# Performance work log

Measured on AMD Instinct MI355X. Metric: run time of the kernel, lower is better.

## Reference

```python
import jax, jax.numpy as jnp
import numpy as np

N = 50000
NEG_SLOPE = 0.2


def add_self_loops(edge_index, n):
    loops = jnp.arange(n, dtype=edge_index.dtype)
    return jnp.concatenate([edge_index, jnp.stack([loops, loops])], axis=1)


def gat_layer(x, edge_index, W, a_src, a_dst, b, heads, ch):
    # x: [N, F_in], W: [F_in, heads*ch], a_src/a_dst: [heads, ch], b: [heads*ch]
    n = x.shape[0]
    src, dst = edge_index[0], edge_index[1]
    h = (x @ W).reshape(n, heads, ch)                      # [N, H, C]
    alpha_src = jnp.sum(h * a_src, axis=-1)                # [N, H]
    alpha_dst = jnp.sum(h * a_dst, axis=-1)                # [N, H]
    e = jax.nn.leaky_relu(alpha_src[src] + alpha_dst[dst], NEG_SLOPE)  # [E, H]
    # segment softmax over incoming edges of each destination node
    m = jax.ops.segment_max(e, dst, num_segments=n)        # [N, H]
    ex = jnp.exp(e - m[dst])                               # [E, H]
    denom = jax.ops.segment_sum(ex, dst, num_segments=n)   # [N, H]
    alpha = ex / (denom[dst] + 1e-16)                      # [E, H]
    msg = h[src] * alpha[:, :, None]                       # [E, H, C]
    out = jax.ops.segment_sum(msg, dst, num_segments=n)    # [N, H, C]
    return out.reshape(n, heads * ch) + b


def setup_inputs() -> dict:
    key = jax.random.key(0)
    ks = jax.random.split(key, 12)
    input_dim, hidden_dim, output_dim, heads = 128, 32, 64, 4
    E = 1600000
    x = jax.random.normal(ks[0], (N, input_dim), dtype=jnp.float32)
    edge_index = jax.random.randint(ks[1], (2, E), 0, N, dtype=jnp.int64)
    s1 = 1.0 / np.sqrt(input_dim)
    s2 = 1.0 / np.sqrt(hidden_dim * heads)
    W1 = jax.random.uniform(ks[2], (input_dim, heads * hidden_dim), jnp.float32, -s1, s1)
    a_src1 = jax.random.uniform(ks[3], (heads, hidden_dim), jnp.float32, -s1, s1)
    a_dst1 = jax.random.uniform(ks[4], (heads, hidden_dim), jnp.float32, -s1, s1)
    b1 = jnp.zeros((heads * hidden_dim,), jnp.float32)
    W2 = jax.random.uniform(ks[5], (heads * hidden_dim, output_dim), jnp.float32, -s2, s2)
    a_src2 = jax.random.uniform(ks[6], (1, output_dim), jnp.float32, -s2, s2)
    a_dst2 = jax.random.uniform(ks[7], (1, output_dim), jnp.float32, -s2, s2)
    b2 = jnp.zeros((output_dim,), jnp.float32)
    return {"x": x, "edge_index": edge_index,
            "W1": W1, "a_src1": a_src1, "a_dst1": a_dst1, "b1": b1,
            "W2": W2, "a_src2": a_src2, "a_dst2": a_dst2, "b2": b2}


def reference(x, edge_index, W1, a_src1, a_dst1, b1, W2, a_src2, a_dst2, b2):
    n = x.shape[0]
    ei = add_self_loops(edge_index, n)
    h = gat_layer(x, ei, W1, a_src1, a_dst1, b1, heads=4, ch=32)
    h = jax.nn.relu(h)
    out = gat_layer(h, ei, W2, a_src2, a_dst2, b2, heads=1, ch=64)
    return out
```

## Files before the change

kernel.cpp:

```cpp
#include <hip/hip_runtime.h>
#include <hip/hip_bf16.h>
#include <hip/hip_fp16.h>


#define LRELU_SLOPE 0.2f
#define NBMAX 200
#define NBLK  512
#define BCAP  16384
#define CAPIMG 16384

typedef _Float16 f16x8 __attribute__((ext_vector_type(8)));
typedef float f32x4 __attribute__((ext_vector_type(4)));


__global__ __launch_bounds__(256) void hist_kernel(const int* __restrict__ ei_dst,
                                                   int* __restrict__ hist, int E, int chunk) {
    __shared__ int h[NBMAX];
    int t = threadIdx.x;
    for (int i = t; i < NBMAX; i += 256) h[i] = 0;
    __syncthreads();
    int begin = blockIdx.x * chunk;
    int endE = min(E, begin + chunk);
    for (int e = begin + t; e < endE; e += 256) atomicAdd(&h[ei_dst[e] >> 8], 1);
    __syncthreads();
    for (int i = t; i < NBMAX; i += 256) hist[i * NBLK + blockIdx.x] = h[i];
}

__global__ __launch_bounds__(512) void bucket_scan_kernel(int* __restrict__ hist,
                                                          int* __restrict__ gfill) {
    __shared__ int buf[2][NBLK];
    int b = blockIdx.x, t = threadIdx.x;
    buf[0][t] = hist[b * NBLK + t];
    __syncthreads();
    int pi = 0;
#pragma unroll
    for (int off = 1; off < NBLK; off <<= 1) {
        int v = buf[pi][t];
        if (t >= off) v += buf[pi][t - off];
        buf[pi ^ 1][t] = v;
        __syncthreads();
        pi ^= 1;
    }
    hist[b * NBLK + t] = (t == 0) ? 0 : buf[pi][t - 1];
    if (t == 0) gfill[b] = buf[pi][NBLK - 1];
}

__global__ __launch_bounds__(256) void scatter2_kernel(const int* __restrict__ ei_src,
                                                       const int* __restrict__ ei_dst,
                                                       const int* __restrict__ hist,
                                                       unsigned int* __restrict__ records,
                                                       int E, int chunk) {
    __shared__ int base[NBMAX];
    __shared__ int lcnt[NBMAX];
    int t = threadIdx.x;
    for (int i = t; i < NBMAX; i += 256) {
        base[i] = hist[i * NBLK + blockIdx.x];
        lcnt[i] = 0;
    }
    __syncthreads();
    int begin = blockIdx.x * chunk;
    int endE = min(E, begin + chunk);
    for (int e = begin + t; e < endE; e += 256) {
        int s = ei_src[e], d = ei_dst[e];
        int bkt = d >> 8;
        unsigned int rec = (unsigned int)d | ((unsigned int)s << 16);
        int r = atomicAdd(&lcnt[bkt], 1);
        records[(size_t)bkt * BCAP + base[bkt] + r] = rec;
    }
}

__global__ __launch_bounds__(256) void scan_blocksums_kernel(const int* __restrict__ gfill,
                                                             int* __restrict__ bsums,
                                                             int* __restrict__ row_ptr,
                                                             int nblocks, int n, int total) {
    __shared__ int buf[2][256];
    int t = threadIdx.x;
    int v0 = 0;
    if (t < nblocks) v0 = gfill[t] + min(256, n - (t << 8));
    buf[0][t] = v0;
    __syncthreads();
    int pi = 0;
#pragma unroll
    for (int off = 1; off < 256; off <<= 1) {
        int v = buf[pi][t];
        if (t >= off) v += buf[pi][t - off];
        buf[pi ^ 1][t] = v;
        __syncthreads();
        pi ^= 1;
    }
    if (t < nblocks) bsums[t] = (t == 0) ? 0 : buf[pi][t - 1];
    if (t == 0) row_ptr[n] = total;
}

__global__ __launch_bounds__(256) void csr_build_kernel(const unsigned int* __restrict__ records,
                                                        const int* __restrict__ gfill,
                                                        const int* __restrict__ bsums,
                                                        int* __restrict__ row_ptr,
                                                        unsigned short* __restrict__ col,
                                                        int N) {
    __shared__ int cnt[256];
    __shared__ int buf[2][256];
    __shared__ unsigned short img[CAPIMG];
    __shared__ int lfill[256];
    int t = threadIdx.x, b = blockIdx.x;
    int gi = (b << 8) + t;
    bool valid = gi < N;
    cnt[t] = valid ? 1 : 0;
    __syncthreads();
    int c = gfill[b];
    const unsigned int* r = records + (size_t)b * BCAP;
    for (int i = t; i < c; i += 256) atomicAdd(&cnt[r[i] & 255], 1);
    __syncthreads();
    int d = cnt[t];
    buf[0][t] = d;
    __syncthreads();
    int pi = 0;
#pragma unroll
    for (int off = 1; off < 256; off <<= 1) {
        int v = buf[pi][t];
        if (t >= off) v += buf[pi][t - off];
        buf[pi ^ 1][t] = v;
        __syncthreads();
        pi ^= 1;
    }
    int rbase = bsums[b];
    int nvalid = min(256, N - (b << 8));
    int size = c + max(nvalid, 0);
    bool lds = (size <= CAPIMG);
    if (valid) {
        int local = buf[pi][t] - d;
        row_ptr[gi] = rbase + local;
        lfill[t] = local + 1;
        if (lds) img[local] = (unsigned short)gi;
        else col[rbase + local] = (unsigned short)gi;
    }
    __syncthreads();
    for (int i = t; i < c; i += 256) {
        unsigned int rec = r[i];
        int d8 = rec & 255;
        unsigned short s = (unsigned short)(rec >> 16);
        int p = atomicAdd(&lfill[d8], 1);
        if (lds) img[p] = s;
        else col[rbase + p] = s;
    }
    __syncthreads();
    if (lds) {
        for (int i = t; i < size; i += 256) col[rbase + i] = img[i];
    }
}


__global__ __launch_bounds__(256) void gemm1_mfma_kernel(const float* __restrict__ X,
                                                         const float* __restrict__ W,
                                                         __half* __restrict__ outh,
                                                         const float* __restrict__ a_src,
                                                         const float* __restrict__ a_dst,
                                                         float* __restrict__ as_out,
                                                         float* __restrict__ ad_out, int nrows) {
    constexpr int KP = 136;
    __shared__ _Float16 wlds[128 * KP];
    int t = threadIdx.x;
    int wv = t >> 6, lane = t & 63;
    int quad = lane >> 4, m16 = lane & 15;
    for (int i = t; i < 4096; i += 256) {
        int k = i >> 5;
        int n0 = (i & 31) << 2;
        float4 v = *(const float4*)(W + k * 128 + n0);
        wlds[(n0 + 0) * KP + k] = (_Float16)v.x;
        wlds[(n0 + 1) * KP + k] = (_Float16)v.y;
        wlds[(n0 + 2) * KP + k] = (_Float16)v.z;
        wlds[(n0 + 3) * KP + k] = (_Float16)v.w;
    }
    __syncthreads();

    int row = blockIdx.x * 64 + wv * 16 + m16;
    int rowC = min(row, nrows - 1);
    const float* xp = X + (size_t)rowC * 128;

    f32x4 acc[8];
#pragma unroll
    for (int nt = 0; nt < 8; ++nt) acc[nt] = (f32x4)0.f;

    for (int kt = 0; kt < 128; kt += 32) {
        float4 v0 = *(const float4*)(xp + kt + quad * 8);
        float4 v1 = *(const float4*)(xp + kt + quad * 8 + 4);
        f16x8 af;
        af[0] = (_Float16)v0.x; af[1] = (_Float16)v0.y;
        af[2] = (_Float16)v0.z; af[3] = (_Float16)v0.w;
        af[4] = (_Float16)v1.x; af[5] = (_Float16)v1.y;
        af[6] = (_Float16)v1.z; af[7] = (_Float16)v1.w;
#pragma unroll
        for (int nt = 0; nt < 8; ++nt) {
            f16x8 bf = *(const f16x8*)(&wlds[(nt * 16 + m16) * KP + kt + quad * 8]);
            acc[nt] = __builtin_amdgcn_mfma_f32_16x16x32_f16(af, bf, acc[nt], 0, 0, 0);
        }
    }

    float aS[8], aD[8];
#pragma unroll
    for (int nt = 0; nt < 8; ++nt) {
        aS[nt] = a_src[nt * 16 + m16];
        aD[nt] = a_dst[nt * 16 + m16];
    }
    int rowBaseW = blockIdx.x * 64 + wv * 16;
#pragma unroll
    for (int r = 0; r < 4; ++r) {
        int orow = rowBaseW + quad * 4 + r;
        bool ov = orow < nrows;
        if (ov) {
#pragma unroll
            for (int nt = 0; nt < 8; ++nt)
                outh[(size_t)orow * 128 + nt * 16 + m16] = __float2half(acc[nt][r]);
        }
#pragma unroll
        for (int h = 0; h < 4; ++h) {
            float ss = acc[2 * h][r] * aS[2 * h] + acc[2 * h + 1][r] * aS[2 * h + 1];
            float dd = acc[2 * h][r] * aD[2 * h] + acc[2 * h + 1][r] * aD[2 * h + 1];
#pragma unroll
            for (int o = 1; o < 16; o <<= 1) {
                ss += __shfl_xor(ss, o, 64);
                dd += __shfl_xor(dd, o, 64);
            }
            if (ov && m16 == h) {
                as_out[orow * 4 + h] = ss;
                ad_out[orow * 4 + h] = dd;
            }
        }
    }
}


__global__ __launch_bounds__(256) void gemm2_mfma_kernel(const __half* __restrict__ Xh,
                                                         const float* __restrict__ W,
                                                         __half* __restrict__ outh,
                                                         const float* __restrict__ a_src,
                                                         const float* __restrict__ a_dst,
                                                         float* __restrict__ as_out,
                                                         float* __restrict__ ad_out, int nrows) {
    constexpr int KP = 136;
    __shared__ _Float16 wlds[64 * KP];
    int t = threadIdx.x;
    int wv = t >> 6, lane = t & 63;
    int quad = lane >> 4, m16 = lane & 15;
    for (int i = t; i < 2048; i += 256) {
        int k = i >> 4;
        int n0 = (i & 15) << 2;
        float4 v = *(const float4*)(W + k * 64 + n0);
        wlds[(n0 + 0) * KP + k] = (_Float16)v.x;
        wlds[(n0 + 1) * KP + k] = (_Float16)v.y;
        wlds[(n0 + 2) * KP + k] = (_Float16)v.z;
        wlds[(n0 + 3) * KP + k] = (_Float16)v.w;
    }
    __syncthreads();

    int row = blockIdx.x * 64 + wv * 16 + m16;
    int rowC = min(row, nrows - 1);
    const _Float16* xp = (const _Float16*)Xh + (size_t)rowC * 128;

    f32x4 acc[4];
#pragma unroll
    for (int nt = 0; nt < 4; ++nt) acc[nt] = (f32x4)0.f;

    for (int kt = 0; kt < 128; kt += 32) {
        f16x8 af = *(const f16x8*)(xp + kt + quad * 8);
#pragma unroll
        for (int nt = 0; nt < 4; ++nt) {
            f16x8 bf = *(const f16x8*)(&wlds[(nt * 16 + m16) * KP + kt + quad * 8]);
            acc[nt] = __builtin_amdgcn_mfma_f32_16x16x32_f16(af, bf, acc[nt], 0, 0, 0);
        }
    }

    float aS[4], aD[4];
#pragma unroll
    for (int nt = 0; nt < 4; ++nt) {
        aS[nt] = a_src[nt * 16 + m16];
        aD[nt] = a_dst[nt * 16 + m16];
    }
    int rowBaseW = blockIdx.x * 64 + wv * 16;
#pragma unroll
    for (int r = 0; r < 4; ++r) {
        int orow = rowBaseW + quad * 4 + r;
        bool ov = orow < nrows;
        if (ov) {
#pragma unroll
            for (int nt = 0; nt < 4; ++nt)
                outh[(size_t)orow * 64 + nt * 16 + m16] = __float2half(acc[nt][r]);
        }
        float ss = 0.f, dd = 0.f;
#pragma unroll
        for (int nt = 0; nt < 4; ++nt) {
            ss = fmaf(acc[nt][r], aS[nt], ss);
            dd = fmaf(acc[nt][r], aD[nt], dd);
        }
#pragma unroll
        for (int o = 1; o < 16; o <<= 1) {
            ss += __shfl_xor(ss, o, 64);
            dd += __shfl_xor(dd, o, 64);
        }
        if (ov && m16 == 0) {
            as_out[orow] = ss;
            ad_out[orow] = dd;
        }
    }
}


__global__ __launch_bounds__(256) void agg1_kernel(const __half* __restrict__ h1h,
                                                   const float* __restrict__ asrc,
                                                   const float* __restrict__ adst,
                                                   const int* __restrict__ row_ptr,
                                                   const unsigned short* __restrict__ col,
                                                   const float* __restrict__ b1,
                                                   __half* __restrict__ out, int n) {
    int wave = threadIdx.x >> 6;
    int lane = threadIdx.x & 63;
    int node = blockIdx.x * 4 + wave;
    if (node >= n) return;
    int g = lane >> 4;
    int c16 = lane & 15;
    int headA = c16 >> 2;
    int hp1 = lane & 3;
    int j16 = lane >> 2;
    float ad1 = adst[node * 4 + hp1];
    int start = row_ptr[node], end = row_ptr[node + 1];
    float acc[8];
#pragma unroll
    for (int k = 0; k < 8; ++k) acc[k] = 0.f;
    float s = 0.f;
    const _Float16* hp = (const _Float16*)h1h;
    for (int base = start; base < end; base += 64) {
        int idx = base + lane;
        int cnt = min(64, end - base);
        int myS = (idx < end) ? (int)col[idx] : 0;
        float pr[4];
#pragma unroll
        for (int e = 0; e < 4; ++e) {
            int j = e * 16 + j16;
            int srcj = __shfl(myS, j, 64);
            float ev = asrc[srcj * 4 + hp1] + ad1;
            ev = (ev > 0.f) ? ev : LRELU_SLOPE * ev;
            pr[e] = (j < cnt) ? __expf(ev) : 0.f;
        }
#pragma unroll
        for (int e = 0; e < 4; ++e) {
            int ebase = e << 4;
            if (ebase < cnt) {
                float pre = pr[e];
                int lim = min(ebase + 16, cnt);
                for (int j0 = ebase; j0 < lim; j0 += 4) {
                    int edge = j0 + g;
                    unsigned src = (unsigned)__shfl(myS, edge, 64);
                    float p = __shfl(pre, ((edge & 15) << 2) + headA, 64);
                    f16x8 hv = *(const f16x8*)(hp + ((size_t)src << 7) + (c16 << 3));
#pragma unroll
                    for (int k = 0; k < 8; ++k) acc[k] = fmaf(p, (float)hv[k], acc[k]);
                    s += p;
                }
            }
        }
    }
    s += __shfl_xor(s, 16, 64);
    s += __shfl_xor(s, 32, 64);
#pragma unroll
    for (int k = 0; k < 8; ++k) {
        acc[k] += __shfl_xor(acc[k], 16, 64);
        acc[k] += __shfl_xor(acc[k], 32, 64);
    }
    if (g == 0) {
        float inv = 1.f / (s + 1e-16f);
        float4 bb0 = ((const float4*)b1)[c16 * 2];
        float4 bb1 = ((const float4*)b1)[c16 * 2 + 1];
        f16x8 o;
        o[0] = (_Float16)fmaxf(acc[0] * inv + bb0.x, 0.f);
        o[1] = (_Float16)fmaxf(acc[1] * inv + bb0.y, 0.f);
        o[2] = (_Float16)fmaxf(acc[2] * inv + bb0.z, 0.f);
        o[3] = (_Float16)fmaxf(acc[3] * inv + bb0.w, 0.f);
        o[4] = (_Float16)fmaxf(acc[4] * inv + bb1.x, 0.f);
        o[5] = (_Float16)fmaxf(acc[5] * inv + bb1.y, 0.f);
        o[6] = (_Float16)fmaxf(acc[6] * inv + bb1.z, 0.f);
        o[7] = (_Float16)fmaxf(acc[7] * inv + bb1.w, 0.f);
        *(f16x8*)((_Float16*)out + ((size_t)node << 7) + (c16 << 3)) = o;
    }
}

__global__ __launch_bounds__(256) void agg2_kernel(const __half* __restrict__ h2bh,
                                                   const float* __restrict__ asrc,
                                                   const float* __restrict__ adst,
                                                   const int* __restrict__ row_ptr,
                                                   const unsigned short* __restrict__ col,
                                                   const float* __restrict__ b2,
                                                   float* __restrict__ out, int n) {
    int wave = threadIdx.x >> 6;
    int lane = threadIdx.x & 63;
    int node = blockIdx.x * 4 + wave;
    if (node >= n) return;
    int g = lane >> 3;
    int c8 = lane & 7;
    float ad = adst[node];
    int start = row_ptr[node], end = row_ptr[node + 1];
    float acc[8];
#pragma unroll
    for (int k = 0; k < 8; ++k) acc[k] = 0.f;
    float s = 0.f;
    const _Float16* hp = (const _Float16*)h2bh;
    for (int base = start; base < end; base += 64) {
        int idx = base + lane;
        int cnt = min(64, end - base);
        int myS = (idx < end) ? (int)col[idx] : 0;
        float ev = asrc[myS] + ad;
        ev = (ev > 0.f) ? ev : LRELU_SLOPE * ev;
        float pr = (lane < cnt) ? __expf(ev) : 0.f;
        for (int j0 = 0; j0 < cnt; j0 += 8) {
            int edge = j0 + g;
            unsigned src = (unsigned)__shfl(myS, edge, 64);
            float p = __shfl(pr, edge, 64);
            f16x8 hv = *(const f16x8*)(hp + ((size_t)src << 6) + (c8 << 3));
#pragma unroll
            for (int k = 0; k < 8; ++k) acc[k] = fmaf(p, (float)hv[k], acc[k]);
            s += p;
        }
    }
    s += __shfl_xor(s, 8, 64);
    s += __shfl_xor(s, 16, 64);
    s += __shfl_xor(s, 32, 64);
#pragma unroll
    for (int k = 0; k < 8; ++k) {
        acc[k] += __shfl_xor(acc[k], 8, 64);
        acc[k] += __shfl_xor(acc[k], 16, 64);
        acc[k] += __shfl_xor(acc[k], 32, 64);
    }
    if (g == 0) {
        float inv = 1.f / (s + 1e-16f);
        float4 bb0 = ((const float4*)b2)[c8 * 2];
        float4 bb1 = ((const float4*)b2)[c8 * 2 + 1];
        float4 o0, o1;
        o0.x = acc[0] * inv + bb0.x;
        o0.y = acc[1] * inv + bb0.y;
        o0.z = acc[2] * inv + bb0.z;
        o0.w = acc[3] * inv + bb0.w;
        o1.x = acc[4] * inv + bb1.x;
        o1.y = acc[5] * inv + bb1.y;
        o1.z = acc[6] * inv + bb1.z;
        o1.w = acc[7] * inv + bb1.w;
        float* op = out + (size_t)node * 64 + c8 * 8;
        *(float4*)op = o0;
        *(float4*)(op + 4) = o1;
    }
}


extern "C" void kernel_launch(void* const* d_in, const int* in_sizes, int n_in,
                              void* d_out, int out_size, void* d_ws, size_t ws_size,
                              hipStream_t stream) {
    const float* x      = (const float*)d_in[0];
    const int*   ei     = (const int*)d_in[1];
    const float* W1     = (const float*)d_in[2];
    const float* a_src1 = (const float*)d_in[3];
    const float* a_dst1 = (const float*)d_in[4];
    const float* b1     = (const float*)d_in[5];
    const float* W2     = (const float*)d_in[6];
    const float* a_src2 = (const float*)d_in[7];
    const float* a_dst2 = (const float*)d_in[8];
    const float* b2     = (const float*)d_in[9];
    float* out = (float*)d_out;

    const int N = in_sizes[0] / 128;
    const int E = in_sizes[1] / 2;
    const int total = E + N;
    const int nBuckets = (N + 255) >> 8;

    char* ws = (char*)d_ws;
    size_t off = 0;
    auto alloc = [&](size_t bytes) {
        void* p = ws + off;
        off += (bytes + 255) & ~(size_t)255;
        return p;
    };
    float* regionA = (float*)alloc((size_t)N * 128 * 4);
    __half* h1h   = (__half*)alloc((size_t)N * 128 * 2);
    __half* h2bh  = (__half*)alloc((size_t)N * 64 * 2);
    float* asrc1  = (float*)alloc((size_t)N * 4 * 4);
    float* adst1  = (float*)alloc((size_t)N * 4 * 4);
    float* asrc2  = (float*)alloc((size_t)N * 4);
    float* adst2  = (float*)alloc((size_t)N * 4);
    int*   row_ptr= (int*)alloc((size_t)(N + 1) * 4);
    int*   gfill  = (int*)alloc((size_t)nBuckets * 4);
    int*   bsums  = (int*)alloc((size_t)nBuckets * 4);
    unsigned short* col = (unsigned short*)alloc((size_t)total * 2);

    unsigned int* records = (unsigned int*)regionA;
    int* hist = (int*)(regionA + (size_t)NBMAX * BCAP);
    __half* h2in = (__half*)regionA;
    (void)ws_size; (void)n_in; (void)out_size;

    const int* ei_src = ei;
    const int* ei_dst = ei + E;

    const int chunk = (E + NBLK - 1) / NBLK;
    hist_kernel<<<NBLK, 256, 0, stream>>>(ei_dst, hist, E, chunk);
    bucket_scan_kernel<<<nBuckets, NBLK, 0, stream>>>(hist, gfill);
    scatter2_kernel<<<NBLK, 256, 0, stream>>>(ei_src, ei_dst, hist, records, E, chunk);
    scan_blocksums_kernel<<<1, 256, 0, stream>>>(gfill, bsums, row_ptr, nBuckets, N, total);
    csr_build_kernel<<<nBuckets, 256, 0, stream>>>(records, gfill, bsums, row_ptr, col, N);

    gemm1_mfma_kernel<<<(N + 63) / 64, 256, 0, stream>>>(x, W1, h1h, a_src1, a_dst1,
                                                         asrc1, adst1, N);
    agg1_kernel<<<(N + 3) / 4, 256, 0, stream>>>(h1h, asrc1, adst1,
                                                 row_ptr, col, b1, h2in, N);

    gemm2_mfma_kernel<<<(N + 63) / 64, 256, 0, stream>>>(h2in, W2, h2bh, a_src2, a_dst2,
                                                         asrc2, adst2, N);
    agg2_kernel<<<(N + 3) / 4, 256, 0, stream>>>(h2bh, asrc2, adst2,
                                                 row_ptr, col, b2, out, N);
}
```

Baseline: 253.3 us.

## Partition layer-1 aggregation into source-range passes for cache locality

```diff
diff --git a/kernel.cpp b/kernel.cpp
--- a/kernel.cpp
+++ b/kernel.cpp
@@ -8,6 +8,7 @@
 #define NBLK  512
 #define BCAP  16384
 #define CAPIMG 16384
+#define SRCSH 14
 
 typedef _Float16 f16x8 __attribute__((ext_vector_type(8)));
 typedef float f32x4 __attribute__((ext_vector_type(4)));
@@ -72,6 +73,7 @@
 __global__ __launch_bounds__(256) void scan_blocksums_kernel(const int* __restrict__ gfill,
                                                              int* __restrict__ bsums,
                                                              int* __restrict__ row_ptr,
+                                                             int* __restrict__ rp2,
                                                              int nblocks, int n, int total) {
     __shared__ int buf[2][256];
     int t = threadIdx.x;
@@ -89,57 +91,77 @@
         pi ^= 1;
     }
     if (t < nblocks) bsums[t] = (t == 0) ? 0 : buf[pi][t - 1];
-    if (t == 0) row_ptr[n] = total;
+    if (t == 0) {
+        row_ptr[n] = total;
+        rp2[n * 4] = total;
+    }
 }
 
 __global__ __launch_bounds__(256) void csr_build_kernel(const unsigned int* __restrict__ records,
                                                         const int* __restrict__ gfill,
                                                         const int* __restrict__ bsums,
                                                         int* __restrict__ row_ptr,
+                                                        int* __restrict__ rp2,
                                                         unsigned short* __restrict__ col,
                                                         int N) {
-    __shared__ int cnt[256];
-    __shared__ int buf[2][256];
+    __shared__ int cnt2[1024];
+    __shared__ int tsum[2][256];
     __shared__ unsigned short img[CAPIMG];
-    __shared__ int lfill[256];
     int t = threadIdx.x, b = blockIdx.x;
     int gi = (b << 8) + t;
     bool valid = gi < N;
-    cnt[t] = valid ? 1 : 0;
-    __syncthreads();
+    for (int i = t; i < 1024; i += 256) cnt2[i] = 0;
+    __syncthreads();
+    if (valid) atomicAdd(&cnt2[(t << 2) + (gi >> SRCSH)], 1);
     int c = gfill[b];
     const unsigned int* r = records + (size_t)b * BCAP;
-    for (int i = t; i < c; i += 256) atomicAdd(&cnt[r[i] & 255], 1);
-    __syncthreads();
-    int d = cnt[t];
-    buf[0][t] = d;
+    for (int i = t; i < c; i += 256) {
+        unsigned int rec = r[i];
+        atomicAdd(&cnt2[((rec & 255) << 2) + ((rec >> 16) >> SRCSH)], 1);
+    }
+    __syncthreads();
+    int l0 = cnt2[t * 4 + 0], l1 = cnt2[t * 4 + 1];
+    int l2 = cnt2[t * 4 + 2], l3 = cnt2[t * 4 + 3];
+    int mysum = l0 + l1 + l2 + l3;
+    tsum[0][t] = mysum;
     __syncthreads();
     int pi = 0;
 #pragma unroll
     for (int off = 1; off < 256; off <<= 1) {
-        int v = buf[pi][t];
-        if (t >= off) v += buf[pi][t - off];
-        buf[pi ^ 1][t] = v;
+        int v = tsum[pi][t];
+        if (t >= off) v += tsum[pi][t - off];
+        tsum[pi ^ 1][t] = v;
         __syncthreads();
         pi ^= 1;
     }
+    int tbase = tsum[pi][t] - mysum;
+    int e0 = tbase, e1 = e0 + l0, e2 = e1 + l1, e3 = e2 + l2;
     int rbase = bsums[b];
+    if (valid) {
+        row_ptr[gi] = rbase + e0;
+        rp2[gi * 4 + 0] = rbase + e0;
+        rp2[gi * 4 + 1] = rbase + e1;
+        rp2[gi * 4 + 2] = rbase + e2;
+        rp2[gi * 4 + 3] = rbase + e3;
+    }
+    cnt2[t * 4 + 0] = e0;
+    cnt2[t * 4 + 1] = e1;
+    cnt2[t * 4 + 2] = e2;
+    cnt2[t * 4 + 3] = e3;
+    __syncthreads();
     int nvalid = min(256, N - (b << 8));
     int size = c + max(nvalid, 0);
     bool lds = (size <= CAPIMG);
     if (valid) {
-        int local = buf[pi][t] - d;
-        row_ptr[gi] = rbase + local;
-        lfill[t] = local + 1;
-        if (lds) img[local] = (unsigned short)gi;
-        else col[rbase + local] = (unsigned short)gi;
-    }
-    __syncthreads();
+        int p = atomicAdd(&cnt2[(t << 2) + (gi >> SRCSH)], 1);
+        if (lds) img[p] = (unsigned short)gi;
+        else col[rbase + p] = (unsigned short)gi;
+    }
     for (int i = t; i < c; i += 256) {
         unsigned int rec = r[i];
-        int d8 = rec & 255;
+        int idx = ((rec & 255) << 2) + ((rec >> 16) >> SRCSH);
         unsigned short s = (unsigned short)(rec >> 16);
-        int p = atomicAdd(&lfill[d8], 1);
+        int p = atomicAdd(&cnt2[idx], 1);
         if (lds) img[p] = s;
         else col[rbase + p] = s;
     }
@@ -305,24 +327,28 @@
 }
 
 
-__global__ __launch_bounds__(256) void agg1_kernel(const __half* __restrict__ h1h,
-                                                   const float* __restrict__ asrc,
-                                                   const float* __restrict__ adst,
-                                                   const int* __restrict__ row_ptr,
-                                                   const unsigned short* __restrict__ col,
-                                                   const float* __restrict__ b1,
-                                                   __half* __restrict__ out, int n) {
+__global__ __launch_bounds__(256) void agg1_pass_kernel(const __half* __restrict__ h1h,
+                                                        const float* __restrict__ asrc,
+                                                        const float* __restrict__ adst,
+                                                        const int* __restrict__ rp2,
+                                                        const unsigned short* __restrict__ col,
+                                                        const float* __restrict__ b1,
+                                                        __half* __restrict__ accbuf,
+                                                        float* __restrict__ s_acc,
+                                                        int n, int pass) {
     int wave = threadIdx.x >> 6;
     int lane = threadIdx.x & 63;
     int node = blockIdx.x * 4 + wave;
     if (node >= n) return;
+    int start = rp2[node * 4 + pass];
+    int end = rp2[node * 4 + pass + 1];
+    if (start == end && (pass == 1 || pass == 2)) return;
     int g = lane >> 4;
     int c16 = lane & 15;
     int headA = c16 >> 2;
     int hp1 = lane & 3;
     int j16 = lane >> 2;
     float ad1 = adst[node * 4 + hp1];
-    int start = row_ptr[node], end = row_ptr[node + 1];
     float acc[8];
 #pragma unroll
     for (int k = 0; k < 8; ++k) acc[k] = 0.f;
@@ -366,22 +392,40 @@
         acc[k] += __shfl_xor(acc[k], 16, 64);
         acc[k] += __shfl_xor(acc[k], 32, 64);
     }
-    if (g == 0) {
-        float inv = 1.f / (s + 1e-16f);
+    if (g != 0) return;
+    _Float16* ap = (_Float16*)accbuf + ((size_t)node << 7) + (c16 << 3);
+    if (pass == 0) {
+        f16x8 o;
+#pragma unroll
+        for (int k = 0; k < 8; ++k) o[k] = (_Float16)acc[k];
+        *(f16x8*)ap = o;
+        if ((c16 & 3) == 0) s_acc[node * 4 + headA] = s;
+    } else if (pass < 3) {
+        f16x8 pv = *(const f16x8*)ap;
+        f16x8 o;
+#pragma unroll
+        for (int k = 0; k < 8; ++k) o[k] = (_Float16)(acc[k] + (float)pv[k]);
+        *(f16x8*)ap = o;
+        if ((c16 & 3) == 0) s_acc[node * 4 + headA] += s;
+    } else {
+        float stot = s_acc[node * 4 + headA] + s;
+        float inv = 1.f / (stot + 1e-16f);
+        f16x8 pv = *(const f16x8*)ap;
         float4 bb0 = ((const float4*)b1)[c16 * 2];
         float4 bb1 = ((const float4*)b1)[c16 * 2 + 1];
         f16x8 o;
-        o[0] = (_Float16)fmaxf(acc[0] * inv + bb0.x, 0.f);
-        o[1] = (_Float16)fmaxf(acc[1] * inv + bb0.y, 0.f);
-        o[2] = (_Float16)fmaxf(acc[2] * inv + bb0.z, 0.f);
-        o[3] = (_Float16)fmaxf(acc[3] * inv + bb0.w, 0.f);
-        o[4] = (_Float16)fmaxf(acc[4] * inv + bb1.x, 0.f);
-        o[5] = (_Float16)fmaxf(acc[5] * inv + bb1.y, 0.f);
-        o[6] = (_Float16)fmaxf(acc[6] * inv + bb1.z, 0.f);
-        o[7] = (_Float16)fmaxf(acc[7] * inv + bb1.w, 0.f);
-        *(f16x8*)((_Float16*)out + ((size_t)node << 7) + (c16 << 3)) = o;
-    }
-}
+        o[0] = (_Float16)fmaxf((acc[0] + (float)pv[0]) * inv + bb0.x, 0.f);
+        o[1] = (_Float16)fmaxf((acc[1] + (float)pv[1]) * inv + bb0.y, 0.f);
+        o[2] = (_Float16)fmaxf((acc[2] + (float)pv[2]) * inv + bb0.z, 0.f);
+        o[3] = (_Float16)fmaxf((acc[3] + (float)pv[3]) * inv + bb0.w, 0.f);
+        o[4] = (_Float16)fmaxf((acc[4] + (float)pv[4]) * inv + bb1.x, 0.f);
+        o[5] = (_Float16)fmaxf((acc[5] + (float)pv[5]) * inv + bb1.y, 0.f);
+        o[6] = (_Float16)fmaxf((acc[6] + (float)pv[6]) * inv + bb1.z, 0.f);
+        o[7] = (_Float16)fmaxf((acc[7] + (float)pv[7]) * inv + bb1.w, 0.f);
+        *(f16x8*)ap = o;
+    }
+}
+
 
 __global__ __launch_bounds__(256) void agg2_kernel(const __half* __restrict__ h2bh,
                                                    const float* __restrict__ asrc,
@@ -483,7 +527,9 @@
     float* adst1  = (float*)alloc((size_t)N * 4 * 4);
     float* asrc2  = (float*)alloc((size_t)N * 4);
     float* adst2  = (float*)alloc((size_t)N * 4);
+    float* s_acc  = (float*)alloc((size_t)N * 4 * 4);
     int*   row_ptr= (int*)alloc((size_t)(N + 1) * 4);
+    int*   rp2    = (int*)alloc((size_t)(N * 4 + 1) * 4);
     int*   gfill  = (int*)alloc((size_t)nBuckets * 4);
     int*   bsums  = (int*)alloc((size_t)nBuckets * 4);
     unsigned short* col = (unsigned short*)alloc((size_t)total * 2);
@@ -500,13 +546,15 @@
     hist_kernel<<<NBLK, 256, 0, stream>>>(ei_dst, hist, E, chunk);
     bucket_scan_kernel<<<nBuckets, NBLK, 0, stream>>>(hist, gfill);
     scatter2_kernel<<<NBLK, 256, 0, stream>>>(ei_src, ei_dst, hist, records, E, chunk);
-    scan_blocksums_kernel<<<1, 256, 0, stream>>>(gfill, bsums, row_ptr, nBuckets, N, total);
-    csr_build_kernel<<<nBuckets, 256, 0, stream>>>(records, gfill, bsums, row_ptr, col, N);
+    scan_blocksums_kernel<<<1, 256, 0, stream>>>(gfill, bsums, row_ptr, rp2, nBuckets, N, total);
+    csr_build_kernel<<<nBuckets, 256, 0, stream>>>(records, gfill, bsums, row_ptr, rp2, col, N);
 
     gemm1_mfma_kernel<<<(N + 63) / 64, 256, 0, stream>>>(x, W1, h1h, a_src1, a_dst1,
                                                          asrc1, adst1, N);
-    agg1_kernel<<<(N + 3) / 4, 256, 0, stream>>>(h1h, asrc1, adst1,
-                                                 row_ptr, col, b1, h2in, N);
+    for (int pass = 0; pass < 4; ++pass) {
+        agg1_pass_kernel<<<(N + 3) / 4, 256, 0, stream>>>(h1h, asrc1, adst1, rp2, col, b1,
+                                                          h2in, s_acc, N, pass);
+    }
 
     gemm2_mfma_kernel<<<(N + 63) / 64, 256, 0, stream>>>(h2in, W2, h2bh, a_src2, a_dst2,
                                                          asrc2, adst2, N);
```

After: 298.7 us. 1.18x slower.
